# Kernel optimization log

Hardware: AMD Instinct MI355X
Metric: run time of the kernel (lower is better)

The kernel has to match this reference:

```python
import jax, jax.numpy as jnp
import numpy as np

B, T, D_IN, H, D = 4, 4096, 1024, 16, 64


def setup_inputs() -> dict:
    key = jax.random.key(0)
    k1, k2, k3 = jax.random.split(key, 3)
    inputs = jax.random.normal(k1, (B, T, D_IN), dtype=jnp.float32)
    kv_kernel = jax.random.normal(k2, (D_IN, H, D, 2), dtype=jnp.float32) * (1.0 / np.sqrt(D_IN))
    q_kernel = jax.random.normal(k3, (H, D), dtype=jnp.float32) * (1.0 / np.sqrt(D))
    return {"inputs": inputs, "kv_kernel": kv_kernel, "q_kernel": q_kernel}


def _associate(a, b):
    # Online-softmax combine on packed tuples [m(1), u(1), w(D)] along last axis.
    ma, ua, wa = a[..., :1], a[..., 1:2], a[..., 2:]
    mb, ub, wb = b[..., :1], b[..., 1:2], b[..., 2:]
    m = jnp.maximum(ma, mb)
    ea = jnp.exp(ma - m)
    eb = jnp.exp(mb - m)
    u = ua * ea + ub * eb
    w = wa * ea + wb * eb
    return jnp.concatenate([m, u, w], axis=-1)


def reference(inputs, kv_kernel, q_kernel):
    # inputs: (B,T,D_in); kv_kernel: (D_in,H,D,2); q_kernel: (H,D)
    kv = jnp.einsum('bti,ihdk->bthdk', inputs, kv_kernel)
    kv = jax.nn.relu(kv)  # activation; dropout disabled (inference)
    k = kv[..., 0]  # (B,T,H,D)
    v = kv[..., 1]  # (B,T,H,D)
    st = jnp.einsum('hd,bthd->bth', q_kernel, k)[..., None]  # (B,T,H,1)
    u_init = jnp.ones_like(st)  # exp(s - m) with m = s
    elems = jnp.concatenate([st, u_init, v], axis=-1)  # (B,T,H,D+2)
    o = jax.lax.associative_scan(_associate, elems, axis=1)
    c = o[..., 1:2]  # running denominator
    a = o[..., 2:]   # running numerator (B,T,H,D)
    h = a / c
    # concat_heads=False -> sum over heads
    return jnp.sum(h, axis=-2)  # (B,T,D)
```

## Files before the change

kernel.cpp:

```cpp
#include <hip/hip_runtime.h>
#include <hip/hip_bf16.h>
#include <math.h>

#define B_   4
#define T_   4096
#define DIN_ 1024
#define H_   16
#define D_   64
#define M_   (B_*T_)
#define N_   (H_*D_*2)
#define K_   DIN_
#define C_   64
#define CL_  (T_/C_)

typedef unsigned short u16;
typedef __attribute__((ext_vector_type(8))) short short8_t;
typedef __attribute__((ext_vector_type(4))) float float4_t;

__device__ __forceinline__ u16 f2bf(float f) {
  unsigned int x = __float_as_uint(f);
  x += 0x7fffu + ((x >> 16) & 1u);
  return (u16)(x >> 16);
}
__device__ __forceinline__ float bf2f(unsigned int u) {
  return __uint_as_float((u & 0xffffu) << 16);
}
__device__ __forceinline__ unsigned pk_bf16(float x, float y) {
  float2 f; f.x = x; f.y = y;
  union { __hip_bfloat162 h2; unsigned u; } c;
  c.h2 = __float22bfloat162_rn(f);
  return c.u;
}

__device__ __forceinline__ void g2l16(const u16* g, u16* l) {
  __builtin_amdgcn_global_load_lds(
      (const __attribute__((address_space(1))) void*)g,
      (__attribute__((address_space(3))) void*)l, 16, 0, 0);
}

__global__ __launch_bounds__(256)
void prep(const float* __restrict__ inputs, const float* __restrict__ kvk,
          u16* __restrict__ aB, u16* __restrict__ wBt) {
  __shared__ float tile[32][33];
  int bid = blockIdx.x;
  int tid = threadIdx.x;
  if (bid < 8192) {
    int i = bid * 256 + tid;
    const float4* src = (const float4*)inputs;
    float4 a = src[2*i], b = src[2*i+1];
    uint4 o;
    o.x = pk_bf16(a.x, a.y);
    o.y = pk_bf16(a.z, a.w);
    o.z = pk_bf16(b.x, b.y);
    o.w = pk_bf16(b.z, b.w);
    ((uint4*)aB)[i] = o;
  } else {
    int b2 = bid - 8192;
    int kb = (b2 & 31) * 32;
    int nb = (b2 >> 5) * 32;
    int r  = tid >> 3;
    int c4 = (tid & 7) * 4;
    float4 v = *(const float4*)&kvk[(size_t)(kb + r) * N_ + nb + c4];
    tile[r][c4+0] = v.x; tile[r][c4+1] = v.y; tile[r][c4+2] = v.z; tile[r][c4+3] = v.w;
    __syncthreads();
    uint2 o;
    o.x = pk_bf16(tile[c4+0][r], tile[c4+1][r]);
    o.y = pk_bf16(tile[c4+2][r], tile[c4+3][r]);
    *(uint2*)&wBt[(size_t)(nb + r) * K_ + kb + c4] = o;
  }
}

__global__ __launch_bounds__(256)
void gemm_kv(const u16* __restrict__ A, const u16* __restrict__ Bt,
             const float* __restrict__ q,
             float* __restrict__ pbuf, u16* __restrict__ vbuf,
             float* __restrict__ aggU, float* __restrict__ aggW) {
  __shared__ __align__(16) char smem[33536];
  u16*   lA    = (u16*)smem;
  u16*   lB    = (u16*)(smem + 16384);
  u16*   vtile = (u16*)smem;
  float* sred  = (float*)(smem + 18432);
  float* qs    = (float*)(smem + 32768);
  float* pS    = (float*)(smem + 33024);

  const int tid  = threadIdx.x;
  const int wave = tid >> 6;
  const int lane = tid & 63;
  const int quad = lane >> 4;
  const int l16  = lane & 15;

  const int g    = blockIdx.x;
  const int xcd  = g & 7;
  const int slot = g >> 3;
  const int h    = slot & 15;
  const int mt   = (slot >> 4) * 8 + xcd;
  const int bm = mt * 128;
  const int bn = h * 128;
  const int wm = (wave >> 1) * 64;
  const int wn = (wave & 1) * 64;

  if (tid < D_) qs[tid] = q[h * D_ + tid];

  const int r8 = lane >> 3;
  const int k8 = lane & 7;
  const int gk = (k8 ^ r8) * 8;
  const u16* gaBase = A  + (size_t)(bm + wave*32 + r8) * K_ + gk;
  const u16* gbBase = Bt + (size_t)(bn + wave*32 + r8) * K_ + gk;

  const int fs0 = ((quad    ) ^ (l16 & 7)) * 8;
  const int fs1 = ((quad + 4) ^ (l16 & 7)) * 8;

  float4_t acc[4][4] = {};

  for (int k0 = 0; k0 < K_; k0 += 64) {
    __syncthreads();
#pragma unroll
    for (int call = 0; call < 4; ++call) {
      g2l16(gaBase + k0 + (size_t)(call*8) * K_, lA + (wave*32 + call*8) * 64);
      g2l16(gbBase + k0 + (size_t)(call*8) * K_, lB + (wave*32 + call*8) * 64);
    }
    __syncthreads();

    short8_t af[4][2], bfr[4][2];
#pragma unroll
    for (int i = 0; i < 4; ++i) {
      int row = (wm + i*16 + l16) * 64;
      af[i][0] = *(const short8_t*)&lA[row + fs0];
      af[i][1] = *(const short8_t*)&lA[row + fs1];
    }
#pragma unroll
    for (int j = 0; j < 4; ++j) {
      int row = (wn + j*16 + l16) * 64;
      bfr[j][0] = *(const short8_t*)&lB[row + fs0];
      bfr[j][1] = *(const short8_t*)&lB[row + fs1];
    }
#pragma unroll
    for (int t = 0; t < 2; ++t)
#pragma unroll
      for (int i = 0; i < 4; ++i)
#pragma unroll
        for (int j = 0; j < 4; ++j)
          acc[i][j] = __builtin_amdgcn_mfma_f32_16x16x32_bf16(af[i][t], bfr[j][t], acc[i][j], 0, 0, 0);
  }

  __syncthreads();

  if (l16 & 1) {
#pragma unroll
    for (int j = 0; j < 4; ++j) {
      int d = ((wn + j*16 + l16) & 127) >> 1;
#pragma unroll
      for (int i = 0; i < 4; ++i)
#pragma unroll
        for (int r = 0; r < 4; ++r) {
          int t = wm + i*16 + quad*4 + r;
          vtile[t*72 + d] = f2bf(fmaxf(acc[i][j][r], 0.f));
        }
    }
  } else {
    int slot2 = (wn >> 3) + (l16 >> 1);
#pragma unroll
    for (int i = 0; i < 4; ++i)
#pragma unroll
      for (int r = 0; r < 4; ++r) {
        int t = wm + i*16 + quad*4 + r;
        float p = 0.f;
#pragma unroll
        for (int j = 0; j < 4; ++j) {
          int d = ((wn + j*16 + l16) & 127) >> 1;
          p += qs[d] * fmaxf(acc[i][j][r], 0.f);
        }
        sred[t*17 + slot2] = p;
      }
  }
  __syncthreads();

  const int b   = mt >> 5;
  const int tt0 = (mt & 31) * 128;
  const int bh  = b * H_ + h;

  if (tid < 128) {
    float ssum = 0.f;
#pragma unroll
    for (int k = 0; k < 16; ++k) ssum += sred[tid*17 + k];
    float p = __expf(fminf(fmaxf(ssum, -60.f), 60.f));
    pS[tid] = p;
    pbuf[(size_t)bh * T_ + tt0 + tid] = p;
  }
  __syncthreads();

  if (wave < 2) {
    int d = lane;
    float U = 0.f, W = 0.f;
#pragma unroll 4
    for (int i = 0; i < CL_; ++i) {
      int t = wave * CL_ + i;
      float p = pS[t];
      float v = bf2f(vtile[t*72 + d]);
      U += p;
      W += p * v;
    }
    int blk = bh * C_ + (mt & 31) * 2 + wave;
    aggW[(size_t)blk * D_ + d] = W;
    if (d == 0) aggU[blk] = U;
  } else {
    int idx = tid - 128;
    int d0  = (idx & 7) * 8;
    int tr  = idx >> 3;
    u16* vg = vbuf + ((size_t)bh * T_ + tt0) * D_;
#pragma unroll
    for (int itv = 0; itv < 8; ++itv) {
      int t = tr + 16*itv;
      uint4 val = *(const uint4*)&vtile[t*72 + d0];
      *(uint4*)&vg[(size_t)t * D_ + d0] = val;
    }
  }
}

__global__ __launch_bounds__(1024)
void scan_pass3(const u16* __restrict__ vbuf, const float* __restrict__ pbuf,
                const float* __restrict__ aggU, const float* __restrict__ aggW,
                float* __restrict__ out) {
  __shared__ float pS[H_][CL_];
  __shared__ float wbuf[H_][8][D_ + 1];
  int bc = blockIdx.x;
  int b  = bc >> 6;
  int c  = bc & (C_ - 1);
  int tid  = threadIdx.x;
  int h    = tid >> 6;
  int lane = tid & 63;
  int bh   = b * H_ + h;
  int t0   = c * CL_;

  pS[h][lane] = pbuf[(size_t)bh * T_ + t0 + lane];

  float U = 0.f, W = 0.f;
  for (int j = 0; j < c; ++j) {
    int idx = bh * C_ + j;
    U += aggU[idx];
    W += aggW[(size_t)idx * D_ + lane];
  }
  __syncthreads();

  const u16* vp = vbuf + ((size_t)bh * T_ + t0) * D_ + lane;
  for (int gg = 0; gg < 8; ++gg) {
#pragma unroll
    for (int ii = 0; ii < 8; ++ii) {
      int i = gg * 8 + ii;
      float p = pS[h][i];
      float v = bf2f(vp[i * D_]);
      U += p;
      W += p * v;
      wbuf[h][ii][lane] = __fdividef(W, U);
    }
    __syncthreads();
    if (tid < 512) {
      int ii = tid >> 6, dd = tid & 63;
      float acc = 0.f;
#pragma unroll
      for (int hh = 0; hh < H_; ++hh) acc += wbuf[hh][ii][dd];
      out[((size_t)b * T_ + t0 + gg*8 + ii) * D_ + dd] = acc;
    }
    __syncthreads();
  }
}

extern "C" void kernel_launch(void* const* d_in, const int* in_sizes, int n_in,
                              void* d_out, int out_size, void* d_ws, size_t ws_size,
                              hipStream_t stream) {
  const float* inputs = (const float*)d_in[0];
  const float* kvk    = (const float*)d_in[1];
  const float* qk     = (const float*)d_in[2];
  float* out = (float*)d_out;
  char* ws = (char*)d_ws;

  u16*   aB   = (u16*)ws;
  u16*   wBt  = (u16*)(ws + 33554432);
  u16*   vb   = (u16*)(ws + 37748736);
  float* pb   = (float*)(ws + 71303168);
  float* aggU = (float*)(ws + 72351744);
  float* aggW = (float*)(ws + 72368128);

  prep<<<10240, 256, 0, stream>>>(inputs, kvk, aB, wBt);
  gemm_kv<<<2048, 256, 0, stream>>>(aB, wBt, qk, pb, vb, aggU, aggW);
  scan_pass3<<<B_*C_, 1024, 0, stream>>>(vb, pb, aggU, aggW, out);
}
```

Baseline: 220.1 us.

## Rewrite KV GEMM as 256x256 tile with double-buffered LDS pipeline

Moves the KV projection GEMM from 128x128 tiles with 4 waves to 256x256 tiles with 8 waves. LDS is double-buffered (128KB dynamic), and global-to-LDS loads are interleaved with MFMA quadrants under explicit barriers, vmcnt waits and setprio. The aim is to hide load latency and raise arithmetic intensity. The epilogue is reworked to handle two heads per block, using shuffle-based partial reductions for the score. In exchange it needs much more LDS and registers per block and launches fewer blocks (512).

```diff
diff --git a/kernel.cpp b/kernel.cpp
--- a/kernel.cpp
+++ b/kernel.cpp
@@ -70,149 +70,211 @@
   }
 }
 
-__global__ __launch_bounds__(256)
+
+#define SCB __builtin_amdgcn_sched_barrier(0)
+#define KBAR do { SCB; __builtin_amdgcn_s_barrier(); SCB; } while (0)
+
+#define STAGE_A(P, KT, CC) do { \
+  g2l16(gA + ((size_t)((CC)*64      ) * K_ + (KT)*64), lds + (P)*16384 +        (CC)*4096 + wv*512); \
+  g2l16(gA + ((size_t)((CC)*64 + 128) * K_ + (KT)*64), lds + (P)*16384 + 8192 + (CC)*4096 + wv*512); \
+} while (0)
+
+#define STAGE_B(P, KT, HH) do { \
+  g2l16(gB + ((size_t)((HH)*128     ) * K_ + (KT)*64), lds + 32768 + (P)*16384 + (HH)*8192 +        wv*512); \
+  g2l16(gB + ((size_t)((HH)*128 + 64) * K_ + (KT)*64), lds + 32768 + (P)*16384 + (HH)*8192 + 4096 + wv*512); \
+} while (0)
+
+#define READ_A(P, MH) do { _Pragma("unroll") \
+  for (int il_ = 0; il_ < 4; ++il_) { \
+    const int o_ = (P)*16384 + aBase + (MH)*4096 + il_*1024; \
+    af[il_][0] = *(const short8_t*)&lds[o_ + s0]; \
+    af[il_][1] = *(const short8_t*)&lds[o_ + s1]; \
+  } } while (0)
+
+#define READ_B(P, NH) do { _Pragma("unroll") \
+  for (int jl_ = 0; jl_ < 2; ++jl_) { \
+    const int o_ = (P)*16384 + (NH)*8192 + bBase + jl_*1024; \
+    bfr[NH][jl_][0] = *(const short8_t*)&lds[o_ + s0]; \
+    bfr[NH][jl_][1] = *(const short8_t*)&lds[o_ + s1]; \
+  } } while (0)
+
+#define MFMA_Q(MH, NH) do { \
+  __builtin_amdgcn_s_setprio(1); \
+  _Pragma("unroll") for (int kk_ = 0; kk_ < 2; ++kk_) \
+  _Pragma("unroll") for (int il_ = 0; il_ < 4; ++il_) \
+  _Pragma("unroll") for (int jl_ = 0; jl_ < 2; ++jl_) \
+    acc[(MH)*4+il_][(NH)*2+jl_] = __builtin_amdgcn_mfma_f32_16x16x32_bf16( \
+        af[il_][kk_], bfr[NH][jl_][kk_], acc[(MH)*4+il_][(NH)*2+jl_], 0, 0, 0); \
+  __builtin_amdgcn_s_setprio(0); \
+} while (0)
+
+__global__ __launch_bounds__(512, 2)
 void gemm_kv(const u16* __restrict__ A, const u16* __restrict__ Bt,
              const float* __restrict__ q,
              float* __restrict__ pbuf, u16* __restrict__ vbuf,
              float* __restrict__ aggU, float* __restrict__ aggW) {
-  __shared__ __align__(16) char smem[33536];
-  u16*   lA    = (u16*)smem;
-  u16*   lB    = (u16*)(smem + 16384);
-  u16*   vtile = (u16*)smem;
-  float* sred  = (float*)(smem + 18432);
-  float* qs    = (float*)(smem + 32768);
-  float* pS    = (float*)(smem + 33024);
+  extern __shared__ __align__(16) char smem[];
+  u16* lds = (u16*)smem;
 
   const int tid  = threadIdx.x;
-  const int wave = tid >> 6;
+  const int wv   = tid >> 6;
   const int lane = tid & 63;
   const int quad = lane >> 4;
   const int l16  = lane & 15;
-
-  const int g    = blockIdx.x;
-  const int xcd  = g & 7;
-  const int slot = g >> 3;
-  const int h    = slot & 15;
-  const int mt   = (slot >> 4) * 8 + xcd;
-  const int bm = mt * 128;
-  const int bn = h * 128;
-  const int wm = (wave >> 1) * 64;
-  const int wn = (wave & 1) * 64;
-
-  if (tid < D_) qs[tid] = q[h * D_ + tid];
-
-  const int r8 = lane >> 3;
-  const int k8 = lane & 7;
-  const int gk = (k8 ^ r8) * 8;
-  const u16* gaBase = A  + (size_t)(bm + wave*32 + r8) * K_ + gk;
-  const u16* gbBase = Bt + (size_t)(bn + wave*32 + r8) * K_ + gk;
-
-  const int fs0 = ((quad    ) ^ (l16 & 7)) * 8;
-  const int fs1 = ((quad + 4) ^ (l16 & 7)) * 8;
-
-  float4_t acc[4][4] = {};
-
-  for (int k0 = 0; k0 < K_; k0 += 64) {
-    __syncthreads();
-#pragma unroll
-    for (int call = 0; call < 4; ++call) {
-      g2l16(gaBase + k0 + (size_t)(call*8) * K_, lA + (wave*32 + call*8) * 64);
-      g2l16(gbBase + k0 + (size_t)(call*8) * K_, lB + (wave*32 + call*8) * 64);
-    }
-    __syncthreads();
-
-    short8_t af[4][2], bfr[4][2];
-#pragma unroll
-    for (int i = 0; i < 4; ++i) {
-      int row = (wm + i*16 + l16) * 64;
-      af[i][0] = *(const short8_t*)&lA[row + fs0];
-      af[i][1] = *(const short8_t*)&lA[row + fs1];
-    }
-#pragma unroll
-    for (int j = 0; j < 4; ++j) {
-      int row = (wn + j*16 + l16) * 64;
-      bfr[j][0] = *(const short8_t*)&lB[row + fs0];
-      bfr[j][1] = *(const short8_t*)&lB[row + fs1];
-    }
-#pragma unroll
-    for (int t = 0; t < 2; ++t)
-#pragma unroll
-      for (int i = 0; i < 4; ++i)
-#pragma unroll
-        for (int j = 0; j < 4; ++j)
-          acc[i][j] = __builtin_amdgcn_mfma_f32_16x16x32_bf16(af[i][t], bfr[j][t], acc[i][j], 0, 0, 0);
-  }
-
+  const int wr   = wv >> 2;
+  const int wc   = wv & 3;
+
+  const int g  = blockIdx.x;
+  const int wg = (g & 7) * 64 + (g >> 3);
+  const int nt = wg & 7;
+  const int mt = wg >> 3;
+  const int bm = mt * 256;
+  const int bn = nt * 256;
+
+  const int tr   = tid >> 3;
+  const int gran = tid & 7;
+  const u16* gA = A  + (size_t)(bm + tr) * K_ + ((gran ^ (tr & 7)) * 8);
+  const u16* gB = Bt + (size_t)(bn + tr) * K_ + ((gran ^ (tr & 7)) * 8);
+
+  const int s0 = ((quad    ) ^ (l16 & 7)) * 8;
+  const int s1 = ((quad + 4) ^ (l16 & 7)) * 8;
+  const int aBase = wr * 8192 + l16 * 64;
+  const int bBase = 32768 + wc * 2048 + l16 * 64;
+
+  float4_t acc[8][4] = {};
+  short8_t af[4][2];
+  short8_t bfr[2][2][2];
+
+  STAGE_A(0, 0, 0); STAGE_A(0, 0, 1);
+  STAGE_B(0, 0, 0); STAGE_B(0, 0, 1);
+  STAGE_A(1, 1, 0); STAGE_B(1, 1, 0);
+  asm volatile("s_waitcnt vmcnt(4)" ::: "memory");
+  KBAR;
+
+#pragma unroll 1
+  for (int it = 0; it < 8; ++it) {
+    const int kt1 = 2*it + 1, kt2 = 2*it + 2, kt3 = 2*it + 3;
+    const bool more = (it < 7);
+    READ_A(0, 0); READ_B(0, 0);
+    STAGE_A(1, kt1, 1);
+    KBAR;
+    MFMA_Q(0, 0);
+    KBAR;
+    READ_B(0, 1);
+    STAGE_B(1, kt1, 1);
+    KBAR;
+    MFMA_Q(0, 1);
+    KBAR;
+    READ_A(0, 1);
+    if (more) STAGE_A(0, kt2, 0);
+    KBAR;
+    MFMA_Q(1, 0);
+    KBAR;
+    if (more) STAGE_B(0, kt2, 0);
+    KBAR;
+    MFMA_Q(1, 1);
+    SCB;
+    if (more) asm volatile("s_waitcnt vmcnt(4)" ::: "memory");
+    else      asm volatile("s_waitcnt vmcnt(0)" ::: "memory");
+    KBAR;
+    READ_A(1, 0); READ_B(1, 0);
+    if (more) STAGE_A(0, kt2, 1);
+    KBAR;
+    MFMA_Q(0, 0);
+    KBAR;
+    READ_B(1, 1);
+    if (more) STAGE_B(0, kt2, 1);
+    KBAR;
+    MFMA_Q(0, 1);
+    KBAR;
+    READ_A(1, 1);
+    if (more) STAGE_A(1, kt3, 0);
+    KBAR;
+    MFMA_Q(1, 0);
+    KBAR;
+    if (more) STAGE_B(1, kt3, 0);
+    KBAR;
+    MFMA_Q(1, 1);
+    SCB;
+    if (more) asm volatile("s_waitcnt vmcnt(4)" ::: "memory");
+    KBAR;
+  }
+
+  u16*   vtile = (u16*)smem;
+  float* sred  = (float*)(smem + 73728);
+  float* pS    = (float*)(smem + 108544);
+
+  float qv[2][2];
+#pragma unroll
+  for (int nh = 0; nh < 2; ++nh)
+#pragma unroll
+    for (int jl = 0; jl < 2; ++jl)
+      qv[nh][jl] = q[nt*128 + nh*64 + wc*16 + jl*8 + (l16 >> 1)];
+
+#pragma unroll
+  for (int nh = 0; nh < 2; ++nh) {
+#pragma unroll
+    for (int i = 0; i < 8; ++i) {
+#pragma unroll
+      for (int r = 0; r < 4; ++r) {
+        const int t = wr*128 + i*16 + quad*4 + r;
+        const float x0 = fmaxf(acc[i][nh*2+0][r], 0.f);
+        const float x1 = fmaxf(acc[i][nh*2+1][r], 0.f);
+        if (l16 & 1) {
+          const int d0 = (wc*32 + l16) >> 1;
+          vtile[(nh*256 + t)*72 + d0    ] = f2bf(x0);
+          vtile[(nh*256 + t)*72 + d0 + 8] = f2bf(x1);
+        }
+        float ps = qv[nh][0]*x0 + qv[nh][1]*x1;
+        ps += __shfl_xor(ps, 2);
+        if ((l16 & 3) == 0)
+          sred[(nh*256 + t)*17 + wc*4 + (l16 >> 2)] = ps;
+      }
+    }
+  }
   __syncthreads();
 
-  if (l16 & 1) {
-#pragma unroll
-    for (int j = 0; j < 4; ++j) {
-      int d = ((wn + j*16 + l16) & 127) >> 1;
-#pragma unroll
-      for (int i = 0; i < 4; ++i)
-#pragma unroll
-        for (int r = 0; r < 4; ++r) {
-          int t = wm + i*16 + quad*4 + r;
-          vtile[t*72 + d] = f2bf(fmaxf(acc[i][j][r], 0.f));
-        }
-    }
-  } else {
-    int slot2 = (wn >> 3) + (l16 >> 1);
-#pragma unroll
-    for (int i = 0; i < 4; ++i)
-#pragma unroll
-      for (int r = 0; r < 4; ++r) {
-        int t = wm + i*16 + quad*4 + r;
-        float p = 0.f;
-#pragma unroll
-        for (int j = 0; j < 4; ++j) {
-          int d = ((wn + j*16 + l16) & 127) >> 1;
-          p += qs[d] * fmaxf(acc[i][j][r], 0.f);
-        }
-        sred[t*17 + slot2] = p;
-      }
+  const int b  = mt >> 4;
+  const int t0 = (mt & 15) * 256;
+  {
+    const int hh = tid >> 8;
+    const int t  = tid & 255;
+    float s = 0.f;
+#pragma unroll
+    for (int k = 0; k < 16; ++k) s += sred[(hh*256 + t)*17 + k];
+    float p = __expf(fminf(fmaxf(s, -60.f), 60.f));
+    pS[hh*256 + t] = p;
+    pbuf[(size_t)(b*H_ + nt*2 + hh) * T_ + t0 + t] = p;
   }
   __syncthreads();
 
-  const int b   = mt >> 5;
-  const int tt0 = (mt & 31) * 128;
-  const int bh  = b * H_ + h;
-
-  if (tid < 128) {
-    float ssum = 0.f;
-#pragma unroll
-    for (int k = 0; k < 16; ++k) ssum += sred[tid*17 + k];
-    float p = __expf(fminf(fmaxf(ssum, -60.f), 60.f));
-    pS[tid] = p;
-    pbuf[(size_t)bh * T_ + tt0 + tid] = p;
-  }
-  __syncthreads();
-
-  if (wave < 2) {
-    int d = lane;
+  {
+    const int hh = wv >> 2;
+    const int ch = wv & 3;
     float U = 0.f, W = 0.f;
-#pragma unroll 4
-    for (int i = 0; i < CL_; ++i) {
-      int t = wave * CL_ + i;
-      float p = pS[t];
-      float v = bf2f(vtile[t*72 + d]);
+#pragma unroll 8
+    for (int i2 = 0; i2 < CL_; ++i2) {
+      const int t = ch*CL_ + i2;
+      float p = pS[hh*256 + t];
+      float v = bf2f(vtile[(hh*256 + t)*72 + lane]);
       U += p;
       W += p * v;
     }
-    int blk = bh * C_ + (mt & 31) * 2 + wave;
-    aggW[(size_t)blk * D_ + d] = W;
-    if (d == 0) aggU[blk] = U;
-  } else {
-    int idx = tid - 128;
-    int d0  = (idx & 7) * 8;
-    int tr  = idx >> 3;
-    u16* vg = vbuf + ((size_t)bh * T_ + tt0) * D_;
-#pragma unroll
-    for (int itv = 0; itv < 8; ++itv) {
-      int t = tr + 16*itv;
-      uint4 val = *(const uint4*)&vtile[t*72 + d0];
-      *(uint4*)&vg[(size_t)t * D_ + d0] = val;
+    const int bh  = b*H_ + nt*2 + hh;
+    const int blk = bh*C_ + (mt & 15)*4 + ch;
+    aggW[(size_t)blk * D_ + lane] = W;
+    if (lane == 0) aggU[blk] = U;
+  }
+  {
+    const int rr = tid >> 3;
+    const int d0 = (tid & 7) * 8;
+#pragma unroll
+    for (int k2 = 0; k2 < 8; ++k2) {
+      const int row = rr + 64*k2;
+      const int hh  = row >> 8;
+      const int t   = row & 255;
+      uint4 val = *(const uint4*)&vtile[(hh*256 + t)*72 + d0];
+      *(uint4*)&vbuf[((size_t)(b*H_ + nt*2 + hh) * T_ + t0 + t) * D_ + d0] = val;
     }
   }
 }
@@ -282,6 +344,6 @@
   float* aggW = (float*)(ws + 72368128);
 
   prep<<<10240, 256, 0, stream>>>(inputs, kvk, aB, wBt);
-  gemm_kv<<<2048, 256, 0, stream>>>(aB, wBt, qk, pb, vb, aggU, aggW);
+  gemm_kv<<<512, 512, 131072, stream>>>(aB, wBt, qk, pb, vb, aggU, aggW);
   scan_pass3<<<B_*C_, 1024, 0, stream>>>(vb, pb, aggU, aggW, out);
 }
```

Measured after the change: 204.5 us. 1.08x faster.
